# Kernel tuning notes

Measured on AMD Instinct MI355X. Metric: run time of the kernel, lower is better.

The kernel has to match this reference:

```python
import jax, jax.numpy as jnp
import numpy as np

N = 256
IL_MMI = 0.02      # insertion loss MMI
IMB = 0.01         # imbalance MMI
IL_CR = 0.02       # insertion loss Crossing
CT = 0.01          # cross talk Crossing


def _mmi_matrix():
    # 2x2 MMI: sqrt(1-IL)*[[t, i r],[i r, t]] with t=sqrt((1+imb)/2), r=sqrt((1-imb)/2)
    a = np.sqrt(1.0 - IL_MMI)
    t = np.sqrt((1.0 + IMB) / 2.0)
    r = np.sqrt((1.0 - IMB) / 2.0)
    mmi2 = a * np.array([[t, 1j * r], [1j * r, t]], dtype=np.complex64)
    # block-diagonal over even pairs (0,1),(2,3),...
    return jnp.asarray(np.kron(np.eye(N // 2, dtype=np.complex64), mmi2))


def _crossing_matrix():
    # pairs start at odd index 1; rows 0 and N-1 pass through with amplitude sqrt(1-IL)*sqrt(1-CT)
    a = np.sqrt(1.0 - IL_CR)
    thru = a * np.sqrt(1.0 - CT)
    cr2 = a * np.array([[np.sqrt(CT), 1j * np.sqrt(1.0 - CT)],
                        [1j * np.sqrt(1.0 - CT), np.sqrt(CT)]], dtype=np.complex64)
    M = np.zeros((N, N), dtype=np.complex64)
    M[0, 0] = thru
    for i in range(1, N - 1, 2):
        M[i:i + 2, i:i + 2] = cr2
    if N % 2 == 0:
        M[-1, -1] = thru
    return jnp.asarray(M)


def setup_inputs() -> dict:
    key = jax.random.key(0)
    thetas = jax.random.uniform(key, (N // 2 + 2, N), dtype=jnp.float32) * (2.0 * np.pi)
    return {"thetas": thetas}


def reference(thetas):
    MMI = _mmi_matrix()
    CR = _crossing_matrix()
    phases = jnp.exp(1j * thetas)  # [N//2+2, N] complex64; diag phase-shift layers

    # arch = ht[0] @ I  (diagonal left-multiply == row scaling)
    arch0 = jnp.diag(phases[0])

    def body(arch, ph):
        # one mesh stage with trailing crossing (iterations i = 0 .. N//2-2)
        arch = MMI @ arch
        arch = ph[:, None] * arch      # ht[i+1] @ arch
        arch = MMI @ arch
        arch = CR @ arch
        return arch, None

    arch, _ = jax.lax.scan(body, arch0, phases[1:N // 2])

    # last loop iteration (i = N//2-1): no crossing
    arch = MMI @ arch
    arch = phases[N // 2][:, None] * arch
    arch = MMI @ arch
    # final phase layer ht[N//2+1]
    arch = phases[N // 2 + 1][:, None] * arch
    return arch
```

## Files before the change

kernel.cpp:

```cpp
#include <hip/hip_runtime.h>


__device__ __forceinline__ float dpp_up1(float x) {
    return __int_as_float(__builtin_amdgcn_update_dpp(
        __float_as_int(x), __float_as_int(x), 0x138, 0xf, 0xf, false));
}
__device__ __forceinline__ float dpp_dn1(float x) {
    return __int_as_float(__builtin_amdgcn_update_dpp(
        __float_as_int(x), __float_as_int(x), 0x130, 0xf, 0xf, false));
}

__device__ __forceinline__ void sincos4(float4 th, float sn[4], float cs[4]) {
    __sincosf(th.x, &sn[0], &cs[0]);
    __sincosf(th.y, &sn[1], &cs[1]);
    __sincosf(th.z, &sn[2], &cs[2]);
    __sincosf(th.w, &sn[3], &cs[3]);
}

__global__ __launch_bounds__(64)
void coef_kernel(const float* __restrict__ thetas,
                 float* __restrict__ coefs)
{
    const int s0   = blockIdx.x;
    const int lane = threadIdx.x;

    const float U  = 0.98f * 0.505f;
    const float W  = 0.98f * 0.495f;
    const float Gc = 0.98f * sqrtf(0.505f * 0.495f);

    float4 th = *(const float4*)(thetas + (s0 + 1) * 256 + 4 * lane);
    float s[4], c[4];
    sincos4(th, s, c);

    float4 A, B, C;
    A.x = U * c[0] - W * c[1];   A.y = U * s[0] - W * s[1];
    A.z = U * c[1] - W * c[0];   A.w = U * s[1] - W * s[0];
    B.x = -Gc * (s[0] + s[1]);   B.y = Gc * (c[0] + c[1]);
    B.z = -Gc * (s[2] + s[3]);   B.w = Gc * (c[2] + c[3]);
    C.x = U * c[2] - W * c[3];   C.y = U * s[2] - W * s[3];
    C.z = U * c[3] - W * c[2];   C.w = U * s[3] - W * s[2];

    float4* cp = (float4*)coefs;
    cp[(s0 * 3 + 0) * 64 + lane] = A;
    cp[(s0 * 3 + 1) * 64 + lane] = B;
    cp[(s0 * 3 + 2) * 64 + lane] = C;
}

__global__ __launch_bounds__(64, 1)
void neuropuls_mesh_kernel(const float* __restrict__ thetas,
                           const float* __restrict__ coefs,
                           float* __restrict__ out)
{
    constexpr int N = 256;
    __shared__ float4 cbuf[2][1536];

    const int lane = threadIdx.x;
    const int col  = blockIdx.x;

    const float BT = sqrtf(0.98f * 0.01f);
    const float BR = sqrtf(0.98f * 0.99f);
    const float eT0 = (lane == 0)  ? BR : BT, eR0 = (lane == 0)  ? 0.f : BR;
    const float eT3 = (lane == 63) ? BR : BT, eR3 = (lane == 63) ? 0.f : BR;

    float vr[4] = {0.f, 0.f, 0.f, 0.f};
    float vi[4] = {0.f, 0.f, 0.f, 0.f};

    {
        const float th0 = thetas[col];
        float s0, c0;
        __sincosf(th0, &s0, &c0);
        const int r0 = col - 4 * lane;
        if (0 <= r0 && r0 < 4) { vr[r0] = c0; vi[r0] = s0; }
    }

    float4 A0, B0, C0, A1, B1, C1, A2, B2, C2;

    auto rd2 = [&](int buf, int k) {
        const float4* p = &cbuf[buf][k * 192 + lane];
        A2 = p[0]; B2 = p[64]; C2 = p[128];
    };

    auto mstep = [&]() {
        {
            const float xr = vr[2], xi = vi[2], yr = vr[3], yi = vi[3];
            vr[2] = C0.x * xr - C0.y * xi + B0.z * yr - B0.w * yi;
            vi[2] = C0.x * xi + C0.y * xr + B0.z * yi + B0.w * yr;
            vr[3] = B0.z * xr - B0.w * xi + C0.z * yr - C0.w * yi;
            vi[3] = B0.z * xi + B0.w * xr + C0.z * yi + C0.w * yr;
        }
        {
            const float xr = vr[0], xi = vi[0], yr = vr[1], yi = vi[1];
            vr[0] = A0.x * xr - A0.y * xi + B0.x * yr - B0.y * yi;
            vi[0] = A0.x * xi + A0.y * xr + B0.x * yi + B0.y * yr;
            vr[1] = B0.x * xr - B0.y * xi + A0.z * yr - A0.w * yi;
            vi[1] = B0.x * xi + B0.y * xr + A0.z * yi + A0.w * yr;
        }
    };

    auto crossing = [&]() {
        const float pv3r = dpp_up1(vr[3]);
        const float pv3i = dpp_up1(vi[3]);
        const float nv0r = dpp_dn1(vr[0]);
        const float nv0i = dpp_dn1(vi[0]);
        {
            const float xr = vr[1], xi = vi[1], yr = vr[2], yi = vi[2];
            vr[1] = BT * xr - BR * yi;  vi[1] = BT * xi + BR * yr;
            vr[2] = BT * yr - BR * xi;  vi[2] = BT * yi + BR * xr;
        }
        vr[0] = eT0 * vr[0] - eR0 * pv3i;  vi[0] = eT0 * vi[0] + eR0 * pv3r;
        vr[3] = eT3 * vr[3] - eR3 * nv0i;  vi[3] = eT3 * vi[3] + eR3 * nv0r;
    };

    auto rotate = [&]() {
        A0 = A1; B0 = B1; C0 = C1;
        A1 = A2; B1 = B2; C1 = C2;
    };

    auto issue_chunk = [&](int c) {
        const float4* src = (const float4*)coefs + (c * 24) * 64 + lane;
        float4* dst = &cbuf[c & 1][0];
        #pragma unroll
        for (int j = 0; j < 24; ++j)
            __builtin_amdgcn_global_load_lds(
                (const __attribute__((address_space(1))) void*)(src + j * 64),
                (__attribute__((address_space(3))) void*)(dst + j * 64),
                16, 0, 0);
    };

    issue_chunk(0);
    issue_chunk(1);
    asm volatile("s_waitcnt vmcnt(24)" ::: "memory");
    __builtin_amdgcn_sched_barrier(0);
    {
        const float4* p = &cbuf[0][lane];
        A0 = p[0]; B0 = p[64]; C0 = p[128];
        p = &cbuf[0][192 + lane];
        A1 = p[0]; B1 = p[64]; C1 = p[128];
    }

    for (int c = 0; c < 15; ++c) {
        const int cb = c & 1;
        #pragma unroll
        for (int k = 0; k < 5; ++k) {
            rd2(cb, k + 2);
            mstep(); crossing(); rotate();
        }
        rd2(cb, 7);
        asm volatile("s_waitcnt lgkmcnt(0)" ::: "memory");
        __builtin_amdgcn_sched_barrier(0);
        if (c <= 13) {
            issue_chunk(c + 2);
            asm volatile("s_waitcnt vmcnt(24)" ::: "memory");
        } else {
            asm volatile("s_waitcnt vmcnt(0)" ::: "memory");
        }
        __builtin_amdgcn_sched_barrier(0);
        mstep(); crossing(); rotate();
        rd2(cb ^ 1, 0);
        mstep(); crossing(); rotate();
        rd2(cb ^ 1, 1);
        mstep(); crossing(); rotate();
    }

    #pragma unroll
    for (int k = 0; k < 6; ++k) {
        rd2(1, k + 2);
        mstep(); crossing(); rotate();
    }
    mstep(); crossing(); rotate();
    mstep();

    {
        float4 thF = *(const float4*)(thetas + 129 * N + 4 * lane);
        float sn[4], cs[4];
        sincos4(thF, sn, cs);
        #pragma unroll
        for (int j = 0; j < 4; ++j) {
            float r = vr[j], i = vi[j];
            vr[j] = cs[j] * r - sn[j] * i;
            vi[j] = cs[j] * i + sn[j] * r;
        }
    }

    #pragma unroll
    for (int j = 0; j < 4; ++j) {
        const int idx = (4 * lane + j) * N + col;
        out[idx]         = vr[j];
        out[N * N + idx] = vi[j];
    }
}

extern "C" void kernel_launch(void* const* d_in, const int* in_sizes, int n_in,
                              void* d_out, int out_size, void* d_ws, size_t ws_size,
                              hipStream_t stream)
{
    const float* thetas = (const float*)d_in[0];
    float* out   = (float*)d_out;
    float* coefs = (float*)d_ws;
    (void)in_sizes; (void)n_in; (void)out_size; (void)ws_size;

    coef_kernel<<<dim3(128), dim3(64), 0, stream>>>(thetas, coefs);
    neuropuls_mesh_kernel<<<dim3(256), dim3(64), 0, stream>>>(thetas, coefs, out);
}
```

Baseline: 74.14 us.

## Split mesh stages into two halves and combine with complex GEMM

The serial chain of 128 mesh stages is split into two groups of 64 stages, each applied to an identity-like start in parallel across 512 single-wave blocks, doubling the available parallelism. Each half writes its 256x256 complex transfer matrix to workspace, and a new tiled complex GEMM kernel multiplies the two halves to form the output. This halves the sequential latency of the per-column recurrence at the cost of an extra kernel launch, a full complex matrix multiply, and workspace round-trips.

```diff
diff --git a/kernel.cpp b/kernel.cpp
--- a/kernel.cpp
+++ b/kernel.cpp
@@ -9,7 +9,6 @@
     return __int_as_float(__builtin_amdgcn_update_dpp(
         __float_as_int(x), __float_as_int(x), 0x130, 0xf, 0xf, false));
 }
-
 __device__ __forceinline__ void sincos4(float4 th, float sn[4], float cs[4]) {
     __sincosf(th.x, &sn[0], &cs[0]);
     __sincosf(th.y, &sn[1], &cs[1]);
@@ -47,15 +46,16 @@
 }
 
 __global__ __launch_bounds__(64, 1)
-void neuropuls_mesh_kernel(const float* __restrict__ thetas,
-                           const float* __restrict__ coefs,
-                           float* __restrict__ out)
+void group_kernel(const float* __restrict__ thetas,
+                  const float* __restrict__ coefs,
+                  float* __restrict__ ws)
 {
     constexpr int N = 256;
     __shared__ float4 cbuf[2][1536];
 
+    const int g    = blockIdx.x >> 8;
+    const int col  = blockIdx.x & 255;
     const int lane = threadIdx.x;
-    const int col  = blockIdx.x;
 
     const float BT = sqrtf(0.98f * 0.01f);
     const float BR = sqrtf(0.98f * 0.99f);
@@ -66,37 +66,39 @@
     float vi[4] = {0.f, 0.f, 0.f, 0.f};
 
     {
-        const float th0 = thetas[col];
-        float s0, c0;
-        __sincosf(th0, &s0, &c0);
         const int r0 = col - 4 * lane;
-        if (0 <= r0 && r0 < 4) { vr[r0] = c0; vi[r0] = s0; }
+        if (0 <= r0 && r0 < 4) {
+            if (g == 0) {
+                float s0, c0;
+                __sincosf(thetas[col], &s0, &c0);
+                vr[r0] = c0; vi[r0] = s0;
+            } else {
+                vr[r0] = 1.f;
+            }
+        }
     }
 
     float4 A0, B0, C0, A1, B1, C1, A2, B2, C2;
-
     auto rd2 = [&](int buf, int k) {
         const float4* p = &cbuf[buf][k * 192 + lane];
         A2 = p[0]; B2 = p[64]; C2 = p[128];
     };
-
     auto mstep = [&]() {
         {
             const float xr = vr[2], xi = vi[2], yr = vr[3], yi = vi[3];
-            vr[2] = C0.x * xr - C0.y * xi + B0.z * yr - B0.w * yi;
-            vi[2] = C0.x * xi + C0.y * xr + B0.z * yi + B0.w * yr;
-            vr[3] = B0.z * xr - B0.w * xi + C0.z * yr - C0.w * yi;
-            vi[3] = B0.z * xi + B0.w * xr + C0.z * yi + C0.w * yr;
+            vr[2] = C0.x*xr - C0.y*xi + B0.z*yr - B0.w*yi;
+            vi[2] = C0.x*xi + C0.y*xr + B0.z*yi + B0.w*yr;
+            vr[3] = B0.z*xr - B0.w*xi + C0.z*yr - C0.w*yi;
+            vi[3] = B0.z*xi + B0.w*xr + C0.z*yi + C0.w*yr;
         }
         {
             const float xr = vr[0], xi = vi[0], yr = vr[1], yi = vi[1];
-            vr[0] = A0.x * xr - A0.y * xi + B0.x * yr - B0.y * yi;
-            vi[0] = A0.x * xi + A0.y * xr + B0.x * yi + B0.y * yr;
-            vr[1] = B0.x * xr - B0.y * xi + A0.z * yr - A0.w * yi;
-            vi[1] = B0.x * xi + B0.y * xr + A0.z * yi + A0.w * yr;
-        }
-    };
-
+            vr[0] = A0.x*xr - A0.y*xi + B0.x*yr - B0.y*yi;
+            vi[0] = A0.x*xi + A0.y*xr + B0.x*yi + B0.y*yr;
+            vr[1] = B0.x*xr - B0.y*xi + A0.z*yr - A0.w*yi;
+            vi[1] = B0.x*xi + B0.y*xr + A0.z*yi + A0.w*yr;
+        }
+    };
     auto crossing = [&]() {
         const float pv3r = dpp_up1(vr[3]);
         const float pv3i = dpp_up1(vi[3]);
@@ -104,20 +106,19 @@
         const float nv0i = dpp_dn1(vi[0]);
         {
             const float xr = vr[1], xi = vi[1], yr = vr[2], yi = vi[2];
-            vr[1] = BT * xr - BR * yi;  vi[1] = BT * xi + BR * yr;
-            vr[2] = BT * yr - BR * xi;  vi[2] = BT * yi + BR * xr;
-        }
-        vr[0] = eT0 * vr[0] - eR0 * pv3i;  vi[0] = eT0 * vi[0] + eR0 * pv3r;
-        vr[3] = eT3 * vr[3] - eR3 * nv0i;  vi[3] = eT3 * vi[3] + eR3 * nv0r;
-    };
-
+            vr[1] = BT*xr - BR*yi;  vi[1] = BT*xi + BR*yr;
+            vr[2] = BT*yr - BR*xi;  vi[2] = BT*yi + BR*xr;
+        }
+        vr[0] = eT0*vr[0] - eR0*pv3i;  vi[0] = eT0*vi[0] + eR0*pv3r;
+        vr[3] = eT3*vr[3] - eR3*nv0i;  vi[3] = eT3*vi[3] + eR3*nv0r;
+    };
     auto rotate = [&]() {
         A0 = A1; B0 = B1; C0 = C1;
         A1 = A2; B1 = B2; C1 = C2;
     };
-
+    const int g8 = g * 8;
     auto issue_chunk = [&](int c) {
-        const float4* src = (const float4*)coefs + (c * 24) * 64 + lane;
+        const float4* src = (const float4*)coefs + ((g8 + c) * 24) * 64 + lane;
         float4* dst = &cbuf[c & 1][0];
         #pragma unroll
         for (int j = 0; j < 24; ++j)
@@ -138,7 +139,7 @@
         A1 = p[0]; B1 = p[64]; C1 = p[128];
     }
 
-    for (int c = 0; c < 15; ++c) {
+    for (int c = 0; c < 7; ++c) {
         const int cb = c & 1;
         #pragma unroll
         for (int k = 0; k < 5; ++k) {
@@ -148,7 +149,7 @@
         rd2(cb, 7);
         asm volatile("s_waitcnt lgkmcnt(0)" ::: "memory");
         __builtin_amdgcn_sched_barrier(0);
-        if (c <= 13) {
+        if (c <= 5) {
             issue_chunk(c + 2);
             asm volatile("s_waitcnt vmcnt(24)" ::: "memory");
         } else {
@@ -169,24 +170,90 @@
     }
     mstep(); crossing(); rotate();
     mstep();
-
-    {
+    if (g == 0) crossing();
+
+    if (g == 1) {
         float4 thF = *(const float4*)(thetas + 129 * N + 4 * lane);
         float sn[4], cs[4];
         sincos4(thF, sn, cs);
         #pragma unroll
         for (int j = 0; j < 4; ++j) {
-            float r = vr[j], i = vi[j];
-            vr[j] = cs[j] * r - sn[j] * i;
-            vi[j] = cs[j] * i + sn[j] * r;
-        }
+            const float r = vr[j], i = vi[j];
+            vr[j] = cs[j]*r - sn[j]*i;
+            vi[j] = cs[j]*i + sn[j]*r;
+        }
+    }
+
+    float* base = ws + 98304 + g * 131072;
+    *(float4*)(base + col * 256 + 4 * lane) =
+        make_float4(vr[0], vr[1], vr[2], vr[3]);
+    *(float4*)(base + 65536 + col * 256 + 4 * lane) =
+        make_float4(vi[0], vi[1], vi[2], vi[3]);
+}
+
+__global__ __launch_bounds__(256)
+void cgemm_kernel(const float* __restrict__ ws,
+                  float* __restrict__ out)
+{
+    __shared__ float As_re[32][36], As_im[32][36];
+    __shared__ float Bs_re[32][36], Bs_im[32][36];
+
+    const int t  = threadIdx.x;
+    const int bx = blockIdx.x;
+    const int r0 = (bx & 7) * 32;
+    const int c0 = (bx >> 3) * 32;
+    const int tr = t & 15, tc = t >> 4;
+
+    const float* Am = ws + 98304 + 131072;
+    const float* Bm = ws + 98304;
+
+    float accr[2][2] = {{0.f,0.f},{0.f,0.f}};
+    float acci[2][2] = {{0.f,0.f},{0.f,0.f}};
+
+    for (int k0 = 0; k0 < 256; k0 += 32) {
+        {
+            const int kk = t >> 3, r4 = 4 * (t & 7);
+            const int ga = (k0 + kk) * 256 + r0 + r4;
+            *(float4*)&As_re[kk][r4] = *(const float4*)(Am + ga);
+            *(float4*)&As_im[kk][r4] = *(const float4*)(Am + 65536 + ga);
+        }
+        {
+            const int cc = t & 31, kq = (t >> 5) * 4;
+            const int gb = (c0 + cc) * 256 + k0 + kq;
+            const float4 br = *(const float4*)(Bm + gb);
+            const float4 bi = *(const float4*)(Bm + 65536 + gb);
+            Bs_re[kq + 0][cc] = br.x;  Bs_im[kq + 0][cc] = bi.x;
+            Bs_re[kq + 1][cc] = br.y;  Bs_im[kq + 1][cc] = bi.y;
+            Bs_re[kq + 2][cc] = br.z;  Bs_im[kq + 2][cc] = bi.z;
+            Bs_re[kq + 3][cc] = br.w;  Bs_im[kq + 3][cc] = bi.w;
+        }
+        __syncthreads();
+        #pragma unroll 8
+        for (int kk = 0; kk < 32; ++kk) {
+            const float2 ar = *(const float2*)&As_re[kk][2 * tr];
+            const float2 ai = *(const float2*)&As_im[kk][2 * tr];
+            const float2 br = *(const float2*)&Bs_re[kk][2 * tc];
+            const float2 bi = *(const float2*)&Bs_im[kk][2 * tc];
+            accr[0][0] += ar.x*br.x - ai.x*bi.x;
+            acci[0][0] += ar.x*bi.x + ai.x*br.x;
+            accr[0][1] += ar.x*br.y - ai.x*bi.y;
+            acci[0][1] += ar.x*bi.y + ai.x*br.y;
+            accr[1][0] += ar.y*br.x - ai.y*bi.x;
+            acci[1][0] += ar.y*bi.x + ai.y*br.x;
+            accr[1][1] += ar.y*br.y - ai.y*bi.y;
+            acci[1][1] += ar.y*bi.y + ai.y*br.y;
+        }
+        __syncthreads();
     }
 
     #pragma unroll
-    for (int j = 0; j < 4; ++j) {
-        const int idx = (4 * lane + j) * N + col;
-        out[idx]         = vr[j];
-        out[N * N + idx] = vi[j];
+    for (int i = 0; i < 2; ++i) {
+        #pragma unroll
+        for (int j = 0; j < 2; ++j) {
+            const int idx = (r0 + 2*tr + i) * 256 + (c0 + 2*tc + j);
+            out[idx]         = accr[i][j];
+            out[65536 + idx] = acci[i][j];
+        }
     }
 }
 
@@ -195,10 +262,11 @@
                               hipStream_t stream)
 {
     const float* thetas = (const float*)d_in[0];
-    float* out   = (float*)d_out;
-    float* coefs = (float*)d_ws;
+    float* out = (float*)d_out;
+    float* ws  = (float*)d_ws;
     (void)in_sizes; (void)n_in; (void)out_size; (void)ws_size;
 
-    coef_kernel<<<dim3(128), dim3(64), 0, stream>>>(thetas, coefs);
-    neuropuls_mesh_kernel<<<dim3(256), dim3(64), 0, stream>>>(thetas, coefs, out);
-}
+    coef_kernel <<<dim3(128), dim3(64),  0, stream>>>(thetas, ws);
+    group_kernel<<<dim3(512), dim3(64),  0, stream>>>(thetas, ws, ws);
+    cgemm_kernel<<<dim3(64),  dim3(256), 0, stream>>>(ws, out);
+}
```

Result: slower. 87.25 us (+17.7%).
